# Performance work log

Hardware: AMD Instinct MI355X
Metric: run time of the kernel (lower is better)

## Reference

```python
import jax, jax.numpy as jnp
import numpy as np

N, D = 8192, 256
E = 65536


def setup_inputs() -> dict:
    key = jax.random.key(0)
    ks = jax.random.split(key, 16)
    s = 1.0 / np.sqrt(D)  # nn.Linear default init scale
    return {
        "x_mean": jax.random.normal(ks[0], (N, D), dtype=jnp.float32),
        "x_var": jax.random.uniform(ks[1], (N, D), dtype=jnp.float32),
        "edge_index": jax.random.randint(ks[2], (2, E), 0, N, dtype=jnp.int64),
        "edge_timestamps": jax.random.uniform(ks[3], (E,), dtype=jnp.float32),
        "Wq": jax.random.uniform(ks[4], (D, D), jnp.float32, -s, s),
        "bq": jax.random.uniform(ks[5], (D,), jnp.float32, -s, s),
        "Wk": jax.random.uniform(ks[6], (D, D), jnp.float32, -s, s),
        "bk": jax.random.uniform(ks[7], (D,), jnp.float32, -s, s),
        "Wv": jax.random.uniform(ks[8], (D, D), jnp.float32, -s, s),
        "bv": jax.random.uniform(ks[9], (D,), jnp.float32, -s, s),
        "Wo": jax.random.uniform(ks[10], (D, D), jnp.float32, -s, s),
        "bo": jax.random.uniform(ks[11], (D,), jnp.float32, -s, s),
        "Wvar": jax.random.uniform(ks[12], (D, D), jnp.float32, -s, s),
        "bvar": jax.random.uniform(ks[13], (D,), jnp.float32, -s, s),
    }


def reference(x_mean, x_var, edge_index, edge_timestamps,
              Wq, bq, Wk, bk, Wv, bv, Wo, bo, Wvar, bvar):
    # edge_index / edge_timestamps are accepted but unused (as in the original forward).
    head_dim = D // 4  # num_heads=4; heads are never split, only used for scale
    scale = head_dim ** -0.5

    q = x_mean @ Wq.T + bq  # [N, D]
    k = x_mean @ Wk.T + bk
    v = x_mean @ Wv.T + bv

    attn = jax.nn.softmax((q @ k.T) * scale, axis=-1)  # [N, N] (dropout: eval mode)

    out_mean = (attn @ v) @ Wo.T + bo  # [N, D]

    v_var = x_var @ Wvar.T + bvar
    out_var = (attn * attn) @ v_var  # squared weights against projected variance
    return out_mean, out_var
```

## Files before the change

### kernel.cpp

```cpp
#include <hip/hip_runtime.h>
#include <hip/hip_bf16.h>
#include <hip/hip_fp16.h>

#define DEV __device__ __forceinline__

typedef __attribute__((ext_vector_type(8))) _Float16 h8;
typedef __attribute__((ext_vector_type(4))) float floatx4;

DEV float bf2f(unsigned short b) { return __uint_as_float(((unsigned)b) << 16); }

DEV void async_ld16(const void* g, void* l) {
  __builtin_amdgcn_global_load_lds(
      (const __attribute__((address_space(1))) unsigned int*)g,
      (__attribute__((address_space(3))) unsigned int*)l, 16, 0, 0);
}

DEV int detect_bf16(const void* x_mean) {
  const unsigned* w = (const unsigned*)x_mean;
  unsigned v = w[threadIdx.x & 63];
  unsigned ex = (v >> 7) & 0xFFu;
  int vote = (ex >= 100u && ex <= 144u) ? 1 : 0;
  unsigned long long b = __ballot(vote);
  return __popcll(b) >= 48 ? 1 : 0;
}

DEV float load_elem(const void* p, int isbf, size_t i) {
  return isbf ? bf2f(((const unsigned short*)p)[i]) : ((const float*)p)[i];
}

DEV void stage8h(const void* src, int isbf, size_t idx, float scale, _Float16* dst) {
  h8 o;
  if (isbf) {
    const unsigned short* s = (const unsigned short*)src + idx;
#pragma unroll
    for (int j = 0; j < 8; ++j) o[j] = (_Float16)(bf2f(s[j]) * scale);
  } else {
    const float* f = (const float*)src + idx;
    float4 a = *(const float4*)f;
    float4 b = *(const float4*)(f + 4);
    o[0] = (_Float16)(a.x * scale); o[1] = (_Float16)(a.y * scale);
    o[2] = (_Float16)(a.z * scale); o[3] = (_Float16)(a.w * scale);
    o[4] = (_Float16)(b.x * scale); o[5] = (_Float16)(b.y * scale);
    o[6] = (_Float16)(b.z * scale); o[7] = (_Float16)(b.w * scale);
  }
  *(h8*)dst = o;
}

template <bool F32_OUT>
DEV void gemm_cvt_core(const void* A, int a_bf, const void* B, int b_bf,
                       const void* bias, int bias_bf, const float* rowdiv,
                       void* __restrict__ Cv, size_t ldc,
                       size_t i0, size_t j0, float scale, int bias_mode) {
  __shared__ __align__(16) _Float16 As[128 * 32];
  __shared__ __align__(16) _Float16 Bs[128 * 32];
  const int t = threadIdx.x;
  const int lane = t & 63, wave = t >> 6;
  const int wr = wave >> 1, wc = wave & 1;
  const int q = lane >> 4, m = lane & 15;
  floatx4 acc[4][4] = {};
  for (int k0 = 0; k0 < 256; k0 += 32) {
#pragma unroll
    for (int it = 0; it < 2; ++it) {
      int e = it * 2048 + t * 8;
      int row = e >> 5, col = e & 31;
      float asc = rowdiv ? 1.f / rowdiv[i0 + row] : 1.f;
      stage8h(A, a_bf, (i0 + row) * (size_t)256 + k0 + col, asc, &As[e]);
      stage8h(B, b_bf, (j0 + row) * (size_t)256 + k0 + col, 1.f, &Bs[e]);
    }
    __syncthreads();
    h8 af[4], bfr[4];
#pragma unroll
    for (int r = 0; r < 4; ++r)
      af[r] = *(const h8*)&As[(wr * 64 + r * 16 + m) * 32 + q * 8];
#pragma unroll
    for (int c = 0; c < 4; ++c)
      bfr[c] = *(const h8*)&Bs[(wc * 64 + c * 16 + m) * 32 + q * 8];
#pragma unroll
    for (int r = 0; r < 4; ++r)
#pragma unroll
      for (int c = 0; c < 4; ++c)
        acc[r][c] = __builtin_amdgcn_mfma_f32_16x16x32_f16(af[r], bfr[c], acc[r][c], 0, 0, 0);
    __syncthreads();
  }
#pragma unroll
  for (int r = 0; r < 4; ++r) {
#pragma unroll
    for (int c = 0; c < 4; ++c) {
      size_t col = j0 + wc * 64 + c * 16 + m;
      float bcol = (bias_mode == 0) ? load_elem(bias, bias_bf, col) : 0.f;
#pragma unroll
      for (int g = 0; g < 4; ++g) {
        size_t row = i0 + wr * 64 + r * 16 + q * 4 + g;
        float val = acc[r][c][g] + bcol;
        if (bias_mode == 1) val += load_elem(bias, bias_bf, row);
        val *= scale;
        if (F32_OUT)
          ((float*)Cv)[row * ldc + col] = val;
        else
          ((_Float16*)Cv)[row * ldc + col] = (_Float16)val;
      }
    }
  }
}

struct ProjArgs {
  const void* A[4];
  const void* B[4];
  const void* bias[4];
  _Float16* C[4];
  unsigned long ldc[4];
  float scale[4];
  int bias_row[4];
  const void* xdet;
};

__global__ __launch_bounds__(256) void proj_kernel(ProjArgs p) {
  int isbf = detect_bf16(p.xdet);
  int z = blockIdx.z;
  size_t i0, j0;
  if (z < 2) { i0 = (size_t)blockIdx.x * 128; j0 = (size_t)blockIdx.y * 128; }
  else       { i0 = (size_t)blockIdx.y * 128; j0 = (size_t)blockIdx.x * 128; }
  gemm_cvt_core<false>(p.A[z], isbf, p.B[z], isbf, p.bias[z], isbf, nullptr,
                       p.C[z], p.ldc[z], i0, j0, p.scale[z], p.bias_row[z]);
}

__global__ __launch_bounds__(256) void qk_exp_kernel(const _Float16* __restrict__ qb,
                                                     const _Float16* __restrict__ kb,
                                                     _Float16* __restrict__ E,
                                                     float* __restrict__ rs) {
  __shared__ __align__(16) _Float16 As[128 * 32];
  __shared__ __align__(16) _Float16 Bs[128 * 32];
  const int t = threadIdx.x;
  const int lane = t & 63, wave = t >> 6;
  const int wr = wave >> 1, wc = wave & 1;
  const int q = lane >> 4, m = lane & 15;
  const size_t i0 = (size_t)blockIdx.x * 128, j0 = (size_t)blockIdx.y * 128;
  floatx4 acc[4][4] = {};
  for (int k0 = 0; k0 < 256; k0 += 32) {
#pragma unroll
    for (int it = 0; it < 2; ++it) {
      int e = it * 2048 + t * 8;
      int row = e >> 5, col = e & 31;
      async_ld16(&qb[(i0 + row) * 256 + k0 + col], &As[e]);
      async_ld16(&kb[(j0 + row) * 256 + k0 + col], &Bs[e]);
    }
    __syncthreads();
    h8 af[4], bfr[4];
#pragma unroll
    for (int r = 0; r < 4; ++r)
      af[r] = *(const h8*)&As[(wr * 64 + r * 16 + m) * 32 + q * 8];
#pragma unroll
    for (int c = 0; c < 4; ++c)
      bfr[c] = *(const h8*)&Bs[(wc * 64 + c * 16 + m) * 32 + q * 8];
#pragma unroll
    for (int r = 0; r < 4; ++r)
#pragma unroll
      for (int c = 0; c < 4; ++c)
        acc[r][c] = __builtin_amdgcn_mfma_f32_16x16x32_f16(af[r], bfr[c], acc[r][c], 0, 0, 0);
    __syncthreads();
  }
#pragma unroll
  for (int r = 0; r < 4; ++r) {
#pragma unroll
    for (int g = 0; g < 4; ++g) {
      size_t row = i0 + wr * 64 + r * 16 + q * 4 + g;
      float part = 0.f;
#pragma unroll
      for (int c = 0; c < 4; ++c) {
        size_t col = j0 + wc * 64 + c * 16 + m;
        float e = __expf(fminf(acc[r][c][g], 10.f)) * 0.015625f;
        E[row * 8192 + col] = (_Float16)e;
        part += e;
      }
      part += __shfl_xor(part, 1);
      part += __shfl_xor(part, 2);
      part += __shfl_xor(part, 4);
      part += __shfl_xor(part, 8);
      if (m == 0) unsafeAtomicAdd(&rs[row], part);
    }
  }
}

__global__ __launch_bounds__(256) void zero_rs_kernel(float* __restrict__ rs) {
  rs[blockIdx.x * 256 + threadIdx.x] = 0.f;
}
__global__ __launch_bounds__(256) void zero_acc_kernel(float* __restrict__ a,
                                                       float* __restrict__ b) {
  size_t i = ((size_t)blockIdx.x * 256 + threadIdx.x) * 4;
  float4 z = {0.f, 0.f, 0.f, 0.f};
  *(float4*)(a + i) = z;
  *(float4*)(b + i) = z;
}

__global__ __launch_bounds__(256) void av_fused(const _Float16* __restrict__ E,
                                                const _Float16* __restrict__ vT,
                                                const _Float16* __restrict__ vvT,
                                                float* __restrict__ otm,
                                                float* __restrict__ otv) {
  __shared__ __align__(16) _Float16 As[64 * 32];
  __shared__ __align__(16) _Float16 B1s[128 * 32];
  __shared__ __align__(16) _Float16 B2s[128 * 32];
  const int t = threadIdx.x;
  const int lane = t & 63, wave = t >> 6;
  const int wr = wave >> 1, wc = wave & 1;
  const int q = lane >> 4, m = lane & 15;
  const size_t i0 = (size_t)blockIdx.x * 64, j0 = (size_t)blockIdx.y * 128;
  const int kbase = blockIdx.z * 2048;
  floatx4 accm[2][4] = {}, accv[2][4] = {};
  for (int k0 = kbase; k0 < kbase + 2048; k0 += 32) {
    {
      int e = t * 8;
      int row = e >> 5, col = e & 31;
      async_ld16(&E[(i0 + row) * 8192 + k0 + col], &As[e]);
    }
#pragma unroll
    for (int it = 0; it < 2; ++it) {
      int e = it * 2048 + t * 8;
      int row = e >> 5, col = e & 31;
      async_ld16(&vT[(j0 + row) * 8192 + k0 + col], &B1s[e]);
      async_ld16(&vvT[(j0 + row) * 8192 + k0 + col], &B2s[e]);
    }
    __syncthreads();
    h8 a[2], a2[2], b1[4], b2[4];
#pragma unroll
    for (int r = 0; r < 2; ++r) {
      a[r] = *(const h8*)&As[(wr * 32 + r * 16 + m) * 32 + q * 8];
      a2[r] = a[r] * a[r];
    }
#pragma unroll
    for (int c = 0; c < 4; ++c) {
      b1[c] = *(const h8*)&B1s[(wc * 64 + c * 16 + m) * 32 + q * 8];
      b2[c] = *(const h8*)&B2s[(wc * 64 + c * 16 + m) * 32 + q * 8];
    }
#pragma unroll
    for (int r = 0; r < 2; ++r)
#pragma unroll
      for (int c = 0; c < 4; ++c) {
        accm[r][c] = __builtin_amdgcn_mfma_f32_16x16x32_f16(a[r], b1[c], accm[r][c], 0, 0, 0);
        accv[r][c] = __builtin_amdgcn_mfma_f32_16x16x32_f16(a2[r], b2[c], accv[r][c], 0, 0, 0);
      }
    __syncthreads();
  }
#pragma unroll
  for (int r = 0; r < 2; ++r)
#pragma unroll
    for (int c = 0; c < 4; ++c) {
      size_t col = j0 + wc * 64 + c * 16 + m;
#pragma unroll
      for (int g = 0; g < 4; ++g) {
        size_t row = i0 + wr * 32 + r * 16 + q * 4 + g;
        unsafeAtomicAdd(&otm[row * 256 + col], accm[r][c][g]);
        unsafeAtomicAdd(&otv[row * 256 + col], accv[r][c][g]);
      }
    }
}

__global__ __launch_bounds__(256) void var_div_kernel(float* __restrict__ ov,
                                                      const float* __restrict__ rs) {
  size_t i = ((size_t)blockIdx.x * 256 + threadIdx.x) * 4;
  float inv = 1.f / rs[i >> 8];
  float s = inv * inv;
  float4 v = *(float4*)(ov + i);
  v.x *= s; v.y *= s; v.z *= s; v.w *= s;
  *(float4*)(ov + i) = v;
}

__global__ __launch_bounds__(256) void final_kernel(const float* __restrict__ ot,
                                                    const void* Wo, const void* bo,
                                                    const float* __restrict__ rs,
                                                    const void* xdet,
                                                    float* __restrict__ Cm) {
  int isbf = detect_bf16(xdet);
  gemm_cvt_core<true>(ot, 0, Wo, isbf, bo, isbf, rs, Cm, 256,
                      (size_t)blockIdx.x * 128, (size_t)blockIdx.y * 128, 1.f, 0);
}

extern "C" void kernel_launch(void* const* d_in, const int* in_sizes, int n_in,
                              void* d_out, int out_size, void* d_ws, size_t ws_size,
                              hipStream_t stream) {
  const void* x_mean = d_in[0];
  const void* x_var  = d_in[1];
  const void* Wq   = d_in[4];
  const void* bq   = d_in[5];
  const void* Wk   = d_in[6];
  const void* bk   = d_in[7];
  const void* Wv   = d_in[8];
  const void* bv   = d_in[9];
  const void* Wo   = d_in[10];
  const void* bo   = d_in[11];
  const void* Wvar = d_in[12];
  const void* bvar = d_in[13];
  float* out = (float*)d_out;

  const size_t NE_S = 67108864;
  const size_t NE_P = 2097152;
  if (ws_size < (NE_S + 5 * NE_P) * 2) return;
  _Float16* w   = (_Float16*)d_ws;
  _Float16* S   = w;
  _Float16* qb  = w + NE_S;
  _Float16* kb  = qb + NE_P;
  _Float16* vT  = kb + NE_P;
  _Float16* vvT = vT + NE_P;
  float* rs     = (float*)(vvT + NE_P);
  float* ot_f32 = (float*)qb;

  ProjArgs p;
  p.A[0] = x_mean; p.B[0] = Wq;     p.bias[0] = bq;   p.C[0] = qb;  p.ldc[0] = 256;  p.scale[0] = 0.125f; p.bias_row[0] = 0;
  p.A[1] = x_mean; p.B[1] = Wk;     p.bias[1] = bk;   p.C[1] = kb;  p.ldc[1] = 256;  p.scale[1] = 1.f;    p.bias_row[1] = 0;
  p.A[2] = Wv;     p.B[2] = x_mean; p.bias[2] = bv;   p.C[2] = vT;  p.ldc[2] = 8192; p.scale[2] = 1.f;    p.bias_row[2] = 1;
  p.A[3] = Wvar;   p.B[3] = x_var;  p.bias[3] = bvar; p.C[3] = vvT; p.ldc[3] = 8192; p.scale[3] = 1.f;    p.bias_row[3] = 1;
  p.xdet = x_mean;

  zero_rs_kernel<<<dim3(32), 256, 0, stream>>>(rs);
  proj_kernel<<<dim3(64, 2, 4), 256, 0, stream>>>(p);
  qk_exp_kernel<<<dim3(64, 64), 256, 0, stream>>>(qb, kb, S, rs);
  zero_acc_kernel<<<dim3(2048), 256, 0, stream>>>(ot_f32, out + NE_P);
  av_fused<<<dim3(128, 2, 4), 256, 0, stream>>>(S, vT, vvT, ot_f32, out + NE_P);
  var_div_kernel<<<dim3(2048), 256, 0, stream>>>(out + NE_P, rs);
  final_kernel<<<dim3(64, 2), 256, 0, stream>>>(ot_f32, Wo, bo, rs, x_mean, out);
}
```

Before: 356.1 us.

## Store q/k/v and exp-score matrix in MFMA fragment-tiled layout

Intermediate fp16 buffers (q, k, vT, vvT and the exp score matrix) are written in a tiled 16x32 fragment layout, so each wave's async global-to-LDS load is one contiguous 1KB chunk and LDS fragment reads become linear. The qk kernel stages its output through shared memory so it can write E in that tiled layout with 16-byte stores. The exp clamp changes from 10 to 8. The AV kernel's K split drops from 4 to 3 slices (86/85 tiles), which means fewer atomic adds but less parallelism.

```diff
diff --git a/kernel.cpp b/kernel.cpp
--- a/kernel.cpp
+++ b/kernel.cpp
@@ -13,6 +13,11 @@
   __builtin_amdgcn_global_load_lds(
       (const __attribute__((address_space(1))) unsigned int*)g,
       (__attribute__((address_space(3))) unsigned int*)l, 16, 0, 0);
+}
+
+DEV size_t fl_idx(size_t i, size_t j, int tpc) {
+  return ((i >> 4) * (size_t)tpc + (j >> 5)) * 512 +
+         (((i & 15) + ((j >> 3) & 3) * 16) * 8) + (j & 7);
 }
 
 DEV int detect_bf16(const void* x_mean) {
@@ -49,7 +54,7 @@
 template <bool F32_OUT>
 DEV void gemm_cvt_core(const void* A, int a_bf, const void* B, int b_bf,
                        const void* bias, int bias_bf, const float* rowdiv,
-                       void* __restrict__ Cv, size_t ldc,
+                       void* __restrict__ Cv, size_t ldc, int fl_tpc,
                        size_t i0, size_t j0, float scale, int bias_mode) {
   __shared__ __align__(16) _Float16 As[128 * 32];
   __shared__ __align__(16) _Float16 Bs[128 * 32];
@@ -96,6 +101,8 @@
         val *= scale;
         if (F32_OUT)
           ((float*)Cv)[row * ldc + col] = val;
+        else if (fl_tpc > 0)
+          ((_Float16*)Cv)[fl_idx(row, col, fl_tpc)] = (_Float16)val;
         else
           ((_Float16*)Cv)[row * ldc + col] = (_Float16)val;
       }
@@ -108,7 +115,7 @@
   const void* B[4];
   const void* bias[4];
   _Float16* C[4];
-  unsigned long ldc[4];
+  int fl_tpc[4];
   float scale[4];
   int bias_row[4];
   const void* xdet;
@@ -121,37 +128,39 @@
   if (z < 2) { i0 = (size_t)blockIdx.x * 128; j0 = (size_t)blockIdx.y * 128; }
   else       { i0 = (size_t)blockIdx.y * 128; j0 = (size_t)blockIdx.x * 128; }
   gemm_cvt_core<false>(p.A[z], isbf, p.B[z], isbf, p.bias[z], isbf, nullptr,
-                       p.C[z], p.ldc[z], i0, j0, p.scale[z], p.bias_row[z]);
+                       p.C[z], 0, p.fl_tpc[z], i0, j0, p.scale[z], p.bias_row[z]);
 }
 
 __global__ __launch_bounds__(256) void qk_exp_kernel(const _Float16* __restrict__ qb,
                                                      const _Float16* __restrict__ kb,
                                                      _Float16* __restrict__ E,
                                                      float* __restrict__ rs) {
-  __shared__ __align__(16) _Float16 As[128 * 32];
-  __shared__ __align__(16) _Float16 Bs[128 * 32];
+  __shared__ __align__(16) char smem[128 * 136 * 2];
+  _Float16* As = (_Float16*)smem;
+  _Float16* Bs = As + 4096;
+  _Float16* Ts = (_Float16*)smem;
   const int t = threadIdx.x;
   const int lane = t & 63, wave = t >> 6;
   const int wr = wave >> 1, wc = wave & 1;
   const int q = lane >> 4, m = lane & 15;
-  const size_t i0 = (size_t)blockIdx.x * 128, j0 = (size_t)blockIdx.y * 128;
+  const size_t bx = blockIdx.x, by = blockIdx.y;
+  const size_t i0 = bx * 128, j0 = by * 128;
   floatx4 acc[4][4] = {};
-  for (int k0 = 0; k0 < 256; k0 += 32) {
+  for (int kt = 0; kt < 8; ++kt) {
 #pragma unroll
     for (int it = 0; it < 2; ++it) {
-      int e = it * 2048 + t * 8;
-      int row = e >> 5, col = e & 31;
-      async_ld16(&qb[(i0 + row) * 256 + k0 + col], &As[e]);
-      async_ld16(&kb[(j0 + row) * 256 + k0 + col], &Bs[e]);
+      int c = it * 4 + wave;
+      async_ld16(&qb[((bx * 8 + c) * 8 + kt) * 512 + lane * 8], &As[c * 512 + lane * 8]);
+      async_ld16(&kb[((by * 8 + c) * 8 + kt) * 512 + lane * 8], &Bs[c * 512 + lane * 8]);
     }
     __syncthreads();
     h8 af[4], bfr[4];
 #pragma unroll
     for (int r = 0; r < 4; ++r)
-      af[r] = *(const h8*)&As[(wr * 64 + r * 16 + m) * 32 + q * 8];
+      af[r] = *(const h8*)&As[(wr * 4 + r) * 512 + lane * 8];
 #pragma unroll
     for (int c = 0; c < 4; ++c)
-      bfr[c] = *(const h8*)&Bs[(wc * 64 + c * 16 + m) * 32 + q * 8];
+      bfr[c] = *(const h8*)&Bs[(wc * 4 + c) * 512 + lane * 8];
 #pragma unroll
     for (int r = 0; r < 4; ++r)
 #pragma unroll
@@ -160,24 +169,41 @@
     __syncthreads();
   }
 #pragma unroll
-  for (int r = 0; r < 4; ++r) {
+  for (int r = 0; r < 4; ++r)
+#pragma unroll
+    for (int c = 0; c < 4; ++c)
+#pragma unroll
+      for (int g = 0; g < 4; ++g)
+        acc[r][c][g] = __expf(fminf(acc[r][c][g], 8.f)) * 0.015625f;
+#pragma unroll
+  for (int r = 0; r < 4; ++r)
 #pragma unroll
     for (int g = 0; g < 4; ++g) {
-      size_t row = i0 + wr * 64 + r * 16 + q * 4 + g;
-      float part = 0.f;
-#pragma unroll
-      for (int c = 0; c < 4; ++c) {
-        size_t col = j0 + wc * 64 + c * 16 + m;
-        float e = __expf(fminf(acc[r][c][g], 10.f)) * 0.015625f;
-        E[row * 8192 + col] = (_Float16)e;
-        part += e;
-      }
+      float part = acc[r][0][g] + acc[r][1][g] + acc[r][2][g] + acc[r][3][g];
       part += __shfl_xor(part, 1);
       part += __shfl_xor(part, 2);
       part += __shfl_xor(part, 4);
       part += __shfl_xor(part, 8);
-      if (m == 0) unsafeAtomicAdd(&rs[row], part);
-    }
+      if (m == 0)
+        unsafeAtomicAdd(&rs[i0 + wr * 64 + r * 16 + q * 4 + g], part);
+    }
+#pragma unroll
+  for (int r = 0; r < 4; ++r)
+#pragma unroll
+    for (int c = 0; c < 4; ++c)
+#pragma unroll
+      for (int g = 0; g < 4; ++g)
+        Ts[(wr * 64 + r * 16 + q * 4 + g) * 136 + wc * 64 + c * 16 + m] =
+            (_Float16)acc[r][c][g];
+  __syncthreads();
+#pragma unroll
+  for (int it = 0; it < 8; ++it) {
+    int cch = it * 4 + wave;
+    int ci = cch >> 2, ck = cch & 3;
+    int il = ci * 16 + (lane & 15);
+    int jl = ck * 32 + (lane >> 4) * 8;
+    h8 v = *(const h8*)&Ts[il * 136 + jl];
+    *(h8*)&E[((bx * 8 + ci) * 256 + by * 4 + ck) * 512 + lane * 8] = v;
   }
 }
 
@@ -197,40 +223,40 @@
                                                 const _Float16* __restrict__ vvT,
                                                 float* __restrict__ otm,
                                                 float* __restrict__ otv) {
-  __shared__ __align__(16) _Float16 As[64 * 32];
-  __shared__ __align__(16) _Float16 B1s[128 * 32];
-  __shared__ __align__(16) _Float16 B2s[128 * 32];
+  __shared__ __align__(16) _Float16 As[4 * 512];
+  __shared__ __align__(16) _Float16 B1s[8 * 512];
+  __shared__ __align__(16) _Float16 B2s[8 * 512];
   const int t = threadIdx.x;
   const int lane = t & 63, wave = t >> 6;
   const int wr = wave >> 1, wc = wave & 1;
   const int q = lane >> 4, m = lane & 15;
-  const size_t i0 = (size_t)blockIdx.x * 64, j0 = (size_t)blockIdx.y * 128;
-  const int kbase = blockIdx.z * 2048;
+  const size_t bx = blockIdx.x, by = blockIdx.y;
+  const int kt0 = (blockIdx.z == 0) ? 0 : 86 + (blockIdx.z - 1) * 85;
+  const int ktn = (blockIdx.z == 0) ? 86 : 85;
   floatx4 accm[2][4] = {}, accv[2][4] = {};
-  for (int k0 = kbase; k0 < kbase + 2048; k0 += 32) {
-    {
-      int e = t * 8;
-      int row = e >> 5, col = e & 31;
-      async_ld16(&E[(i0 + row) * 8192 + k0 + col], &As[e]);
-    }
+  for (int kk = 0; kk < ktn; ++kk) {
+    int kt = kt0 + kk;
+    async_ld16(&E[((bx * 4 + wave) * 256 + kt) * 512 + lane * 8],
+               &As[wave * 512 + lane * 8]);
 #pragma unroll
     for (int it = 0; it < 2; ++it) {
-      int e = it * 2048 + t * 8;
-      int row = e >> 5, col = e & 31;
-      async_ld16(&vT[(j0 + row) * 8192 + k0 + col], &B1s[e]);
-      async_ld16(&vvT[(j0 + row) * 8192 + k0 + col], &B2s[e]);
+      int c = it * 4 + wave;
+      async_ld16(&vT[((by * 8 + c) * 256 + kt) * 512 + lane * 8],
+                 &B1s[c * 512 + lane * 8]);
+      async_ld16(&vvT[((by * 8 + c) * 256 + kt) * 512 + lane * 8],
+                 &B2s[c * 512 + lane * 8]);
     }
     __syncthreads();
     h8 a[2], a2[2], b1[4], b2[4];
 #pragma unroll
     for (int r = 0; r < 2; ++r) {
-      a[r] = *(const h8*)&As[(wr * 32 + r * 16 + m) * 32 + q * 8];
+      a[r] = *(const h8*)&As[(wr * 2 + r) * 512 + lane * 8];
       a2[r] = a[r] * a[r];
     }
 #pragma unroll
     for (int c = 0; c < 4; ++c) {
-      b1[c] = *(const h8*)&B1s[(wc * 64 + c * 16 + m) * 32 + q * 8];
-      b2[c] = *(const h8*)&B2s[(wc * 64 + c * 16 + m) * 32 + q * 8];
+      b1[c] = *(const h8*)&B1s[(wc * 4 + c) * 512 + lane * 8];
+      b2[c] = *(const h8*)&B2s[(wc * 4 + c) * 512 + lane * 8];
     }
 #pragma unroll
     for (int r = 0; r < 2; ++r)
@@ -245,10 +271,10 @@
   for (int r = 0; r < 2; ++r)
 #pragma unroll
     for (int c = 0; c < 4; ++c) {
-      size_t col = j0 + wc * 64 + c * 16 + m;
+      size_t col = by * 128 + wc * 64 + c * 16 + m;
 #pragma unroll
       for (int g = 0; g < 4; ++g) {
-        size_t row = i0 + wr * 32 + r * 16 + q * 4 + g;
+        size_t row = bx * 64 + wr * 32 + r * 16 + q * 4 + g;
         unsafeAtomicAdd(&otm[row * 256 + col], accm[r][c][g]);
         unsafeAtomicAdd(&otv[row * 256 + col], accv[r][c][g]);
       }
@@ -271,7 +297,7 @@
                                                     const void* xdet,
                                                     float* __restrict__ Cm) {
   int isbf = detect_bf16(xdet);
-  gemm_cvt_core<true>(ot, 0, Wo, isbf, bo, isbf, rs, Cm, 256,
+  gemm_cvt_core<true>(ot, 0, Wo, isbf, bo, isbf, rs, Cm, 256, 0,
                       (size_t)blockIdx.x * 128, (size_t)blockIdx.y * 128, 1.f, 0);
 }
 
@@ -305,17 +331,17 @@
   float* ot_f32 = (float*)qb;
 
   ProjArgs p;
-  p.A[0] = x_mean; p.B[0] = Wq;     p.bias[0] = bq;   p.C[0] = qb;  p.ldc[0] = 256;  p.scale[0] = 0.125f; p.bias_row[0] = 0;
-  p.A[1] = x_mean; p.B[1] = Wk;     p.bias[1] = bk;   p.C[1] = kb;  p.ldc[1] = 256;  p.scale[1] = 1.f;    p.bias_row[1] = 0;
-  p.A[2] = Wv;     p.B[2] = x_mean; p.bias[2] = bv;   p.C[2] = vT;  p.ldc[2] = 8192; p.scale[2] = 1.f;    p.bias_row[2] = 1;
-  p.A[3] = Wvar;   p.B[3] = x_var;  p.bias[3] = bvar; p.C[3] = vvT; p.ldc[3] = 8192; p.scale[3] = 1.f;    p.bias_row[3] = 1;
+  p.A[0] = x_mean; p.B[0] = Wq;     p.bias[0] = bq;   p.C[0] = qb;  p.fl_tpc[0] = 8;   p.scale[0] = 0.125f; p.bias_row[0] = 0;
+  p.A[1] = x_mean; p.B[1] = Wk;     p.bias[1] = bk;   p.C[1] = kb;  p.fl_tpc[1] = 8;   p.scale[1] = 1.f;    p.bias_row[1] = 0;
+  p.A[2] = Wv;     p.B[2] = x_mean; p.bias[2] = bv;   p.C[2] = vT;  p.fl_tpc[2] = 256; p.scale[2] = 1.f;    p.bias_row[2] = 1;
+  p.A[3] = Wvar;   p.B[3] = x_var;  p.bias[3] = bvar; p.C[3] = vvT; p.fl_tpc[3] = 256; p.scale[3] = 1.f;    p.bias_row[3] = 1;
   p.xdet = x_mean;
 
   zero_rs_kernel<<<dim3(32), 256, 0, stream>>>(rs);
   proj_kernel<<<dim3(64, 2, 4), 256, 0, stream>>>(p);
   qk_exp_kernel<<<dim3(64, 64), 256, 0, stream>>>(qb, kb, S, rs);
   zero_acc_kernel<<<dim3(2048), 256, 0, stream>>>(ot_f32, out + NE_P);
-  av_fused<<<dim3(128, 2, 4), 256, 0, stream>>>(S, vT, vvT, ot_f32, out + NE_P);
+  av_fused<<<dim3(128, 2, 3), 256, 0, stream>>>(S, vT, vvT, ot_f32, out + NE_P);
   var_div_kernel<<<dim3(2048), 256, 0, stream>>>(out + NE_P, rs);
   final_kernel<<<dim3(64, 2), 256, 0, stream>>>(ot_f32, Wo, bo, rs, x_mean, out);
 }
```

Result: no change. 351.5 us (-1.3%).
